# Optimization experiments

Measured on AMD Instinct MI355X. Metric: run time of the kernel, lower is better.

## Reference

```python
import jax, jax.numpy as jnp
import numpy as np

N_NODES = 8000
N_EDGES = 64000
HEADS = 8
OUT_C = 512
NEG_SLOPE = 0.2
EPS = 1e-16


def setup_inputs() -> dict:
    key = jax.random.key(0)
    ks = jax.random.split(key, 8)
    x = jax.random.normal(ks[0], (N_NODES, 128), dtype=jnp.float32)
    edge_index = jax.random.randint(ks[1], (2, N_EDGES), 0, N_NODES, dtype=jnp.int64)
    W_gat = jax.random.normal(ks[2], (128, HEADS * OUT_C), dtype=jnp.float32) * 0.05
    b_gat = jax.random.normal(ks[3], (HEADS * OUT_C,), dtype=jnp.float32) * 0.05
    att_src = jax.random.normal(ks[4], (HEADS, OUT_C), dtype=jnp.float32) * 0.05
    att_dst = jax.random.normal(ks[5], (HEADS, OUT_C), dtype=jnp.float32) * 0.05
    W_lin = jax.random.normal(ks[6], (HEADS * OUT_C, 512), dtype=jnp.float32) * 0.02
    b_lin = jax.random.normal(ks[7], (512,), dtype=jnp.float32) * 0.02
    return {"x": x, "edge_index": edge_index, "W_gat": W_gat, "b_gat": b_gat,
            "att_src": att_src, "att_dst": att_dst, "W_lin": W_lin, "b_lin": b_lin}


def reference(x, edge_index, W_gat, b_gat, att_src, att_dst, W_lin, b_lin):
    N = x.shape[0]
    # shared linear projection (PyG GATConv single-tensor input): [N, H, C]
    h = (x @ W_gat).reshape(N, HEADS, OUT_C)
    # add self loops (PyG default add_self_loops=True)
    loop = jnp.arange(N, dtype=edge_index.dtype)
    src = jnp.concatenate([edge_index[0], loop])  # source j
    dst = jnp.concatenate([edge_index[1], loop])  # destination i
    # per-node attention logits: [N, H]
    a_src = jnp.einsum('nhc,hc->nh', h, att_src)
    a_dst = jnp.einsum('nhc,hc->nh', h, att_dst)
    # edge logits, leaky relu
    e = jax.nn.leaky_relu(a_src[src] + a_dst[dst], NEG_SLOPE)  # [E, H]
    # softmax over edges sharing a destination
    emax = jax.ops.segment_max(e, dst, num_segments=N)
    ez = jnp.exp(e - emax[dst])
    denom = jax.ops.segment_sum(ez, dst, num_segments=N)
    alpha = ez / (denom[dst] + EPS)  # [E, H]
    # weighted scatter-add of source features
    msg = h[src] * alpha[:, :, None]  # [E, H, C]
    agg = jax.ops.segment_sum(msg, dst, num_segments=N)  # [N, H, C]
    gat_out = agg.reshape(N, HEADS * OUT_C) + b_gat
    return gat_out @ W_lin + b_lin
```

## Files before the change

### kernel.cpp

```cpp
#include <hip/hip_runtime.h>
#include <hip/hip_bf16.h>
#include <type_traits>

#define NN   8000
#define NE   64000
#define NE2  72000
#define NH   8
#define OC   512
#define HC   4096
#define KIN  128
#define NOUT 512
#define YW   1024
#define NEG_SLOPE 0.2f

using bf16 = __hip_bfloat16;
typedef float  f32x4  __attribute__((ext_vector_type(4)));
typedef __bf16 bf16x8 __attribute__((ext_vector_type(8)));

static __device__ __forceinline__ void gld_lds16(const bf16* g, bf16* l){
    __builtin_amdgcn_global_load_lds(
        (const __attribute__((address_space(1))) unsigned int*)g,
        (__attribute__((address_space(3))) unsigned int*)l, 16, 0, 0);
}

struct Acc24 { f32x4 a[2][4]; };

static __device__ __forceinline__ void gemm64x128(
    const bf16* __restrict__ A, int lda, const bf16* __restrict__ BT, int ldb,
    int K, bf16* sA, bf16* sB, int tid, Acc24& acc)
{
    const int lane = tid & 63;
    const int w    = tid >> 6;
    const int wm   = w >> 1, wn = w & 1;
    const int m16  = lane & 15, q = lane >> 4;
    const int rA = tid >> 2,  kA = (tid & 3) * 8;
    const int cB0 = tid, cB1 = 256 + tid;
    const int rB0 = cB0 >> 2, kB0 = (cB0 & 3) * 8;
    const int rB1 = cB1 >> 2, kB1 = (cB1 & 3) * 8;
    const size_t gA  = (size_t)rA  * lda + kA;
    const size_t gB0 = (size_t)rB0 * ldb + kB0;
    const size_t gB1 = (size_t)rB1 * ldb + kB1;

    #pragma unroll
    for (int i=0;i<2;++i)
        #pragma unroll
        for (int j=0;j<4;++j)
            #pragma unroll
            for (int r=0;r<4;++r) acc.a[i][j][r] = 0.f;

    gld_lds16(A  + gA,  sA + tid*8);
    gld_lds16(BT + gB0, sB + cB0*8);
    gld_lds16(BT + gB1, sB + cB1*8);
    __syncthreads();

    const int nIter = K / 32;
    for (int it = 0; it < nIter; ++it){
        const int cur = it & 1, nxt = cur ^ 1;
        bf16x8 af[2], bfr[4];
        #pragma unroll
        for (int i=0;i<2;++i)
            af[i]  = *(const bf16x8*)(const void*)(sA + cur*64*32 + ((wm*32 + i*16 + m16)*32 + q*8));
        #pragma unroll
        for (int j=0;j<4;++j)
            bfr[j] = *(const bf16x8*)(const void*)(sB + cur*128*32 + ((wn*64 + j*16 + m16)*32 + q*8));
        if (it + 1 < nIter){
            int ko = (it+1) * 32;
            gld_lds16(A  + gA  + ko, sA + nxt*64*32 + tid*8);
            gld_lds16(BT + gB0 + ko, sB + nxt*128*32 + cB0*8);
            gld_lds16(BT + gB1 + ko, sB + nxt*128*32 + cB1*8);
        }
        #pragma unroll
        for (int i=0;i<2;++i)
            #pragma unroll
            for (int j=0;j<4;++j)
                acc.a[i][j] = __builtin_amdgcn_mfma_f32_16x16x32_bf16(af[i], bfr[j], acc.a[i][j], 0, 0, 0);
        __syncthreads();
    }
}

#define TCVT_NB   2048
#define VSRC_BASE 2048
#define CNT_BASE  2176
#define PHA_NB    2458

__global__ __launch_bounds__(256) void k_phaseA(
    const float* __restrict__ W_lin, const float* __restrict__ b_gat,
    const float* __restrict__ W_gat,
    const float* __restrict__ att_src, const float* __restrict__ att_dst,
    const int* __restrict__ eidx,
    bf16* __restrict__ Wl_t, float* __restrict__ b_eff,
    bf16* __restrict__ Wg_bf, float* __restrict__ v,
    int* __restrict__ counts)
{
    __shared__ __align__(16) float smem[32*33 + 32];
    const int bid = blockIdx.x;
    const int tid = threadIdx.x;

    if (bid < TCVT_NB){
        float (*t)[33] = (float(*)[33])smem;
        float* bpart = smem + 32*33;
        if (tid < 32) bpart[tid] = 0.f;
        __syncthreads();
        int tx = tid & 31, ty = tid >> 5;
        int n0 = (bid & 15) * 32, k0 = (bid >> 4) * 32;
        float pb = 0.f;
        #pragma unroll
        for (int i=0;i<4;++i){
            int k = k0 + ty + 8*i;
            float val = W_lin[(size_t)k*NOUT + n0 + tx];
            t[ty+8*i][tx] = val;
            pb = fmaf(b_gat[k], val, pb);
        }
        atomicAdd(&bpart[tx], pb);
        __syncthreads();
        #pragma unroll
        for (int i=0;i<4;++i)
            Wl_t[(size_t)(n0+ty+8*i)*HC + k0+tx] = __float2bfloat16(t[tx][ty+8*i]);
        if (tid < 32) atomicAdd(b_eff + n0 + tid, bpart[tid]);
    } else if (bid < CNT_BASE){
        int k = bid - VSRC_BASE;
        int lane = tid & 63, g = tid >> 6;
        for (int hh = g; hh < NH; hh += 4){
            const float* wp = W_gat + (size_t)k*HC + hh*OC;
            bf16*        wb = Wg_bf + (size_t)k*HC + hh*OC;
            const float* as = att_src + hh*OC;
            const float* ad = att_dst + hh*OC;
            float ss = 0.f, sd = 0.f;
            #pragma unroll
            for (int c0=0; c0<OC; c0+=64){
                float wv = wp[c0+lane];
                wb[c0+lane] = __float2bfloat16(wv);
                ss = fmaf(wv, as[c0+lane], ss);
                sd = fmaf(wv, ad[c0+lane], sd);
            }
            #pragma unroll
            for (int off=32; off; off>>=1){
                ss += __shfl_down(ss, off);
                sd += __shfl_down(sd, off);
            }
            if (lane == 0){
                v[k*16 + hh]     = ss;
                v[k*16 + 8 + hh] = sd;
            }
        }
    } else {
        int e = (bid - CNT_BASE)*256 + tid;
        if (e < NE2){
            int dst = (e < NE) ? eidx[NE + e] : (e - NE);
            atomicAdd(&counts[dst], 1);
        }
    }
}

__global__ __launch_bounds__(256) void k_phaseB(
    const bf16* __restrict__ Wl_t, const bf16* __restrict__ Wg_bf,
    bf16* __restrict__ WcT,
    const int* __restrict__ counts, int* __restrict__ offsets)
{
    __shared__ __align__(16) char smem_raw[24576];
    __shared__ int part[256];
    const int bid = blockIdx.x;
    const int tid = threadIdx.x;

    if (bid == 64){
        int t = tid;
        int base = t*32;
        int s = 0;
        for (int u=0;u<32;++u){ int i = base+u; if (i<NN) s += counts[i]; }
        part[t] = s;
        __syncthreads();
        for (int off=1; off<256; off<<=1){
            int vv = (t>=off) ? part[t-off] : 0;
            __syncthreads();
            part[t] += vv;
            __syncthreads();
        }
        int run = (t==0) ? 0 : part[t-1];
        for (int u=0;u<32;++u){
            int i = base+u;
            if (i<NN){ offsets[i] = run; run += counts[i]; }
        }
        if (t == 255) offsets[NN] = run;
        return;
    }

    bf16* sA = (bf16*)smem_raw;
    bf16* sB = (bf16*)(smem_raw + 8192);
    const int head = bid >> 3, mt = bid & 7;
    const bf16* A  = Wl_t  + head*OC + (size_t)(mt*64)*HC;
    const bf16* BT = Wg_bf + head*OC;
    Acc24 acc;
    gemm64x128(A, HC, BT, HC, OC, sA, sB, tid, acc);
    const int lane = tid & 63;
    const int w = tid >> 6, wm = w >> 1, wn = w & 1;
    const int m16 = lane & 15, q = lane >> 4;
    #pragma unroll
    for (int i=0;i<2;++i){
        int o_base = mt*64 + wm*32 + i*16 + q*4;
        #pragma unroll
        for (int j=0;j<4;++j){
            int col = head*KIN + wn*64 + j*16 + m16;
            #pragma unroll
            for (int r=0;r<4;++r)
                WcT[(size_t)(o_base + r)*YW + col] = __float2bfloat16(acc.a[i][j][r]);
        }
    }
}

#define FILL_NB 282
#define PHC_NB  782

__global__ __launch_bounds__(256) void k_phaseC(
    const int* __restrict__ eidx, const int* __restrict__ offsets,
    int* __restrict__ cursors, int* __restrict__ esrc,
    const float* __restrict__ x, const float* __restrict__ v,
    float* __restrict__ a_src, float* __restrict__ a_dst)
{
    __shared__ __align__(16) float smem[16*132*2];
    const int bid = blockIdx.x;
    const int tid = threadIdx.x;

    if (bid < FILL_NB){
        int e = bid*256 + tid;
        if (e < NE2){
            int src, dst;
            if (e < NE){ src = eidx[e]; dst = eidx[NE+e]; } else { src = dst = e - NE; }
            int pos = atomicAdd(&cursors[dst], 1);
            esrc[offsets[dst] + pos] = src;
        }
        return;
    }
    float (*xs)[132] = (float(*)[132])smem;
    float (*vt)[132] = (float(*)[132])(smem + 16*132);
    int node0 = (bid - FILL_NB) * 16;
    {
        const float* xg = x + (size_t)node0*KIN;
        int row = tid >> 4, co = (tid & 15) * 8;
        float4 v0 = *(const float4*)(xg + row*KIN + co);
        float4 v1 = *(const float4*)(xg + row*KIN + co + 4);
        *(float4*)&xs[row][co]     = v0;
        *(float4*)&xs[row][co + 4] = v1;
    }
    {
        int base = tid*8;
        #pragma unroll
        for (int j=0;j<8;++j){
            int idx = base + j;
            vt[idx & 15][idx >> 4] = v[idx];
        }
    }
    __syncthreads();
    int ln = tid >> 4, o = tid & 15;
    float acc = 0.f;
    #pragma unroll
    for (int k0=0;k0<KIN;k0+=4){
        float4 xv = *(const float4*)&xs[ln][k0];
        float4 vv = *(const float4*)&vt[o][k0];
        acc += xv.x*vv.x + xv.y*vv.y + xv.z*vv.z + xv.w*vv.w;
    }
    int node = node0 + ln;
    if (o < 8) a_src[node*NH + o]     = acc;
    else       a_dst[node*NH + o - 8] = acc;
}

__global__ __launch_bounds__(256) void k_agg(const int* __restrict__ offs,
    const int* __restrict__ esrc, const float* __restrict__ a_src,
    const float* __restrict__ a_dst, const float* __restrict__ x,
    bf16* __restrict__ Y)
{
    int node = blockIdx.x*4 + (threadIdx.x >> 6);
    int lane = threadIdx.x & 63;
    int s0 = offs[node], s1 = offs[node+1];
    int g = lane >> 3, h = lane & 7;
    float adl = a_dst[node*NH + h];
    float m = -1e30f, sum = 0.f;
    for (int e = s0 + g; e < s1; e += 8){
        float l = a_src[esrc[e]*NH + h] + adl;
        l = l > 0.f ? l : NEG_SLOPE*l;
        float mn = fmaxf(m, l);
        sum = sum*__expf(m - mn) + __expf(l - mn);
        m = mn;
    }
    #pragma unroll
    for (int d=8; d<64; d<<=1){
        float mo = __shfl_xor(m, d);
        float so = __shfl_xor(sum, d);
        float mn = fmaxf(m, mo);
        sum = sum*__expf(m - mn) + so*__expf(mo - mn);
        m = mn;
    }
    float inv = 1.f / (sum + 1e-16f);
    float acc[16];
    #pragma unroll
    for (int j=0;j<16;++j) acc[j] = 0.f;
    for (int s=s0; s<s1; ++s){
        int src = esrc[s];
        float wl = 0.f;
        if (lane < 8){
            float l = a_src[src*NH + lane] + adl;
            l = l > 0.f ? l : NEG_SLOPE*l;
            wl = __expf(l - m) * inv;
        }
        float2 xv = *(const float2*)(x + (size_t)src*KIN + lane*2);
        #pragma unroll
        for (int hh=0; hh<8; ++hh){
            float wh = __shfl(wl, hh);
            acc[hh*2]   = fmaf(wh, xv.x, acc[hh*2]);
            acc[hh*2+1] = fmaf(wh, xv.y, acc[hh*2+1]);
        }
    }
    bf16* yp = Y + (size_t)node*YW + lane*2;
    #pragma unroll
    for (int hh=0; hh<8; ++hh){
        bf16 b0 = __float2bfloat16(acc[hh*2]);
        bf16 b1 = __float2bfloat16(acc[hh*2+1]);
        ushort2 pk;
        pk.x = *(unsigned short*)&b0;
        pk.y = *(unsigned short*)&b1;
        *reinterpret_cast<ushort2*>(yp + hh*KIN) = pk;
    }
}

__global__ __launch_bounds__(256) void k_gemm64(
    const bf16* __restrict__ A, const bf16* __restrict__ BT,
    const float* __restrict__ b_eff, const float* __restrict__ b_lin,
    float* __restrict__ C)
{
    __shared__ __align__(16) char smem_raw[24576];
    bf16* sA = (bf16*)smem_raw;
    bf16* sB = (bf16*)(smem_raw + 8192);
    const int tid = threadIdx.x;
    int m0 = blockIdx.x * 64;
    int n0 = blockIdx.y * 128;
    Acc24 acc;
    gemm64x128(A + (size_t)m0*YW, YW, BT + (size_t)n0*YW, YW, YW, sA, sB, tid, acc);
    const int lane = tid & 63;
    const int w = tid >> 6, wm = w >> 1, wn = w & 1;
    const int m16 = lane & 15, q = lane >> 4;
    #pragma unroll
    for (int i=0;i<2;++i){
        int row_base = m0 + wm*32 + i*16 + q*4;
        #pragma unroll
        for (int j=0;j<4;++j){
            int col = n0 + wn*64 + j*16 + m16;
            float bval = b_eff[col] + b_lin[col];
            #pragma unroll
            for (int r=0;r<4;++r)
                C[(size_t)(row_base + r)*NOUT + col] = acc.a[i][j][r] + bval;
        }
    }
}

extern "C" void kernel_launch(void* const* d_in, const int* in_sizes, int n_in,
                              void* d_out, int out_size, void* d_ws, size_t ws_size,
                              hipStream_t stream)
{
    const float* x       = (const float*)d_in[0];
    const int*   eidx    = (const int*)  d_in[1];
    const float* W_gat   = (const float*)d_in[2];
    const float* b_gat   = (const float*)d_in[3];
    const float* att_src = (const float*)d_in[4];
    const float* att_dst = (const float*)d_in[5];
    const float* W_lin   = (const float*)d_in[6];
    const float* b_lin   = (const float*)d_in[7];
    float* out = (float*)d_out;

    char* p = (char*)d_ws;
    auto alloc = [&](size_t bytes){ void* r = (void*)p; p += (bytes + 255) & ~(size_t)255; return r; };
    bf16*  Wg_bf  = (bf16*) alloc((size_t)KIN*HC*2);
    bf16*  Wl_t   = (bf16*) alloc((size_t)NOUT*HC*2);
    bf16*  WcT    = (bf16*) alloc((size_t)NOUT*YW*2);
    bf16*  Ybuf   = (bf16*) alloc((size_t)NN*YW*2);
    float* v      = (float*)alloc((size_t)KIN*16*4);
    float* a_src  = (float*)alloc((size_t)NN*NH*4);
    float* a_dst  = (float*)alloc((size_t)NN*NH*4);
    int*   offs   = (int*)  alloc((size_t)(NN+1)*4);
    int*   esrc   = (int*)  alloc((size_t)NE2*4);
    int*   counts = (int*)  alloc((size_t)NN*4);
    int*   cursors= (int*)  alloc((size_t)NN*4);
    float* b_eff  = (float*)alloc((size_t)NOUT*4);
    if ((size_t)(p - (char*)d_ws) > ws_size) return;

    hipMemsetAsync(counts, 0, (size_t)2*NN*4 + NOUT*4, stream);
    k_phaseA<<<PHA_NB, 256, 0, stream>>>(W_lin, b_gat, W_gat, att_src, att_dst,
                                         eidx, Wl_t, b_eff, Wg_bf, v, counts);
    k_phaseB<<<65, 256, 0, stream>>>(Wl_t, Wg_bf, WcT, counts, offs);
    k_phaseC<<<PHC_NB, 256, 0, stream>>>(eidx, offs, cursors, esrc, x, v, a_src, a_dst);
    k_agg<<<NN/4, 256, 0, stream>>>(offs, esrc, a_src, a_dst, x, Ybuf);
    k_gemm64<<<dim3(NN/64, NOUT/128), 256, 0, stream>>>(Ybuf, WcT, b_eff, b_lin, out);
}
```

Baseline: 147.5 us.

## Fuse W_lin transpose and bias folding into phase-B weight-combine GEMM

Removes the separate W_lin transpose/bf16 conversion pass (2048 blocks) from phase A. Phase B now reads fp32 W_lin directly, converting and transposing it into LDS inside the GEMM loop. b_gat is appended as row 128 of the bf16 W_gat buffer so the bias contribution b_gat·W_lin falls out of the same GEMM and is atomically added into b_eff. This cuts a full write and re-read of the intermediate transposed weights, at the cost of non-pipelined scalar LDS transposes, bf16 rounding of the bias product, and 96 GEMM blocks each with only 16 k-steps.

Result: no change. 146.7 us (-0.5%).

```diff
diff --git a/kernel.cpp b/kernel.cpp
--- a/kernel.cpp
+++ b/kernel.cpp
@@ -78,51 +78,27 @@
     }
 }
 
-#define TCVT_NB   2048
-#define VSRC_BASE 2048
-#define CNT_BASE  2176
-#define PHA_NB    2458
+#define VSRC_NB   128
+#define BCVT_BASE 128
+#define CNT_BASE  130
+#define PHA_NB    412
 
 __global__ __launch_bounds__(256) void k_phaseA(
-    const float* __restrict__ W_lin, const float* __restrict__ b_gat,
-    const float* __restrict__ W_gat,
+    const float* __restrict__ b_gat, const float* __restrict__ W_gat,
     const float* __restrict__ att_src, const float* __restrict__ att_dst,
     const int* __restrict__ eidx,
-    bf16* __restrict__ Wl_t, float* __restrict__ b_eff,
-    bf16* __restrict__ Wg_bf, float* __restrict__ v,
+    bf16* __restrict__ Wg_ext, float* __restrict__ v,
     int* __restrict__ counts)
 {
-    __shared__ __align__(16) float smem[32*33 + 32];
     const int bid = blockIdx.x;
     const int tid = threadIdx.x;
 
-    if (bid < TCVT_NB){
-        float (*t)[33] = (float(*)[33])smem;
-        float* bpart = smem + 32*33;
-        if (tid < 32) bpart[tid] = 0.f;
-        __syncthreads();
-        int tx = tid & 31, ty = tid >> 5;
-        int n0 = (bid & 15) * 32, k0 = (bid >> 4) * 32;
-        float pb = 0.f;
-        #pragma unroll
-        for (int i=0;i<4;++i){
-            int k = k0 + ty + 8*i;
-            float val = W_lin[(size_t)k*NOUT + n0 + tx];
-            t[ty+8*i][tx] = val;
-            pb = fmaf(b_gat[k], val, pb);
-        }
-        atomicAdd(&bpart[tx], pb);
-        __syncthreads();
-        #pragma unroll
-        for (int i=0;i<4;++i)
-            Wl_t[(size_t)(n0+ty+8*i)*HC + k0+tx] = __float2bfloat16(t[tx][ty+8*i]);
-        if (tid < 32) atomicAdd(b_eff + n0 + tid, bpart[tid]);
-    } else if (bid < CNT_BASE){
-        int k = bid - VSRC_BASE;
+    if (bid < VSRC_NB){
+        int k = bid;
         int lane = tid & 63, g = tid >> 6;
         for (int hh = g; hh < NH; hh += 4){
             const float* wp = W_gat + (size_t)k*HC + hh*OC;
-            bf16*        wb = Wg_bf + (size_t)k*HC + hh*OC;
+            bf16*        wb = Wg_ext + (size_t)k*HC + hh*OC;
             const float* as = att_src + hh*OC;
             const float* ad = att_dst + hh*OC;
             float ss = 0.f, sd = 0.f;
@@ -143,6 +119,14 @@
                 v[k*16 + 8 + hh] = sd;
             }
         }
+    } else if (bid < CNT_BASE){
+        int idx = (bid - BCVT_BASE)*2048 + tid*8;
+        float4 v0 = *(const float4*)(b_gat + idx);
+        float4 v1 = *(const float4*)(b_gat + idx + 4);
+        bf16x8 o;
+        o[0]=(__bf16)v0.x; o[1]=(__bf16)v0.y; o[2]=(__bf16)v0.z; o[3]=(__bf16)v0.w;
+        o[4]=(__bf16)v1.x; o[5]=(__bf16)v1.y; o[6]=(__bf16)v1.z; o[7]=(__bf16)v1.w;
+        *(bf16x8*)(void*)(Wg_ext + (size_t)128*HC + idx) = o;
     } else {
         int e = (bid - CNT_BASE)*256 + tid;
         if (e < NE2){
@@ -152,17 +136,20 @@
     }
 }
 
+#define PB_GEMM_NB 96
+
 __global__ __launch_bounds__(256) void k_phaseB(
-    const bf16* __restrict__ Wl_t, const bf16* __restrict__ Wg_bf,
-    bf16* __restrict__ WcT,
+    const bf16* __restrict__ Wg_ext, const float* __restrict__ W_lin,
+    bf16* __restrict__ WcT, float* __restrict__ b_eff,
     const int* __restrict__ counts, int* __restrict__ offsets)
 {
-    __shared__ __align__(16) char smem_raw[24576];
+    __shared__ __align__(16) bf16 sA[64*32];
+    __shared__ __align__(16) bf16 sB[128*32];
     __shared__ int part[256];
     const int bid = blockIdx.x;
     const int tid = threadIdx.x;
 
-    if (bid == 64){
+    if (bid == PB_GEMM_NB){
         int t = tid;
         int base = t*32;
         int s = 0;
@@ -184,25 +171,81 @@
         return;
     }
 
-    bf16* sA = (bf16*)smem_raw;
-    bf16* sB = (bf16*)(smem_raw + 8192);
-    const int head = bid >> 3, mt = bid & 7;
-    const bf16* A  = Wl_t  + head*OC + (size_t)(mt*64)*HC;
-    const bf16* BT = Wg_bf + head*OC;
-    Acc24 acc;
-    gemm64x128(A, HC, BT, HC, OC, sA, sB, tid, acc);
+    const int head = bid / 12;
+    const int rem  = bid % 12;
+    const int m0   = (rem >> 2) * 64;
+    const int n0   = (rem & 3) * 128;
     const int lane = tid & 63;
     const int w = tid >> 6, wm = w >> 1, wn = w & 1;
     const int m16 = lane & 15, q = lane >> 4;
+
+    const int rA = tid >> 2, kA = (tid & 3) * 8;
+    const int arow = min(m0 + rA, 128);
+    const bf16* Abase = Wg_ext + (size_t)arow*HC + head*OC + kA;
+
+    f32x4 acc[2][4];
+    #pragma unroll
+    for (int i=0;i<2;++i)
+        #pragma unroll
+        for (int j=0;j<4;++j)
+            #pragma unroll
+            for (int r=0;r<4;++r) acc[i][j][r] = 0.f;
+
+    for (int kc = 0; kc < OC; kc += 32){
+        __syncthreads();
+        gld_lds16(Abase + kc, sA + tid*8);
+        #pragma unroll
+        for (int u=0; u<4; ++u){
+            int idx = tid*4 + u;
+            int r    = idx >> 5;
+            int gcol = (idx & 31) * 4;
+            const float* src = W_lin + (size_t)(head*OC + kc + r)*NOUT + n0 + gcol;
+            float4 vv = *(const float4*)src;
+            sB[(gcol+0)*32 + r] = __float2bfloat16(vv.x);
+            sB[(gcol+1)*32 + r] = __float2bfloat16(vv.y);
+            sB[(gcol+2)*32 + r] = __float2bfloat16(vv.z);
+            sB[(gcol+3)*32 + r] = __float2bfloat16(vv.w);
+        }
+        __syncthreads();
+        bf16x8 af[2], bfr[4];
+        #pragma unroll
+        for (int i=0;i<2;++i)
+            af[i]  = *(const bf16x8*)(const void*)(sA + ((wm*32 + i*16 + m16)*32 + q*8));
+        #pragma unroll
+        for (int j=0;j<4;++j)
+            bfr[j] = *(const bf16x8*)(const void*)(sB + ((wn*64 + j*16 + m16)*32 + q*8));
+        #pragma unroll
+        for (int i=0;i<2;++i)
+            #pragma unroll
+            for (int j=0;j<4;++j)
+                acc[i][j] = __builtin_amdgcn_mfma_f32_16x16x32_bf16(af[i], bfr[j], acc[i][j], 0, 0, 0);
+    }
+
     #pragma unroll
     for (int i=0;i<2;++i){
-        int o_base = mt*64 + wm*32 + i*16 + q*4;
+        int row_base = m0 + wm*32 + i*16 + q*4;
         #pragma unroll
         for (int j=0;j<4;++j){
-            int col = head*KIN + wn*64 + j*16 + m16;
-            #pragma unroll
-            for (int r=0;r<4;++r)
-                WcT[(size_t)(o_base + r)*YW + col] = __float2bfloat16(acc.a[i][j][r]);
+            int col = n0 + wn*64 + j*16 + m16;
+            if (row_base + 3 < 128){
+                ushort4 pk;
+                bf16 b0 = __float2bfloat16(acc[i][j][0]);
+                bf16 b1 = __float2bfloat16(acc[i][j][1]);
+                bf16 b2 = __float2bfloat16(acc[i][j][2]);
+                bf16 b3 = __float2bfloat16(acc[i][j][3]);
+                pk.x = *(unsigned short*)&b0; pk.y = *(unsigned short*)&b1;
+                pk.z = *(unsigned short*)&b2; pk.w = *(unsigned short*)&b3;
+                *reinterpret_cast<ushort4*>(WcT + (size_t)col*YW + head*KIN + row_base) = pk;
+            } else {
+                #pragma unroll
+                for (int r=0;r<4;++r){
+                    int row = row_base + r;
+                    if (row < 128)
+                        WcT[(size_t)col*YW + head*KIN + row] = __float2bfloat16(acc[i][j][r]);
+                    else if (row == 128)
+                        atomicAdd(b_eff + col, acc[i][j][r]);
+                }
+            }
         }
     }
 }
@@ -367,8 +410,7 @@
 
     char* p = (char*)d_ws;
     auto alloc = [&](size_t bytes){ void* r = (void*)p; p += (bytes + 255) & ~(size_t)255; return r; };
-    bf16*  Wg_bf  = (bf16*) alloc((size_t)KIN*HC*2);
-    bf16*  Wl_t   = (bf16*) alloc((size_t)NOUT*HC*2);
+    bf16*  Wg_ext = (bf16*) alloc((size_t)129*HC*2);
     bf16*  WcT    = (bf16*) alloc((size_t)NOUT*YW*2);
     bf16*  Ybuf   = (bf16*) alloc((size_t)NN*YW*2);
     float* v      = (float*)alloc((size_t)KIN*16*4);
@@ -382,9 +424,9 @@
     if ((size_t)(p - (char*)d_ws) > ws_size) return;
 
     hipMemsetAsync(counts, 0, (size_t)2*NN*4 + NOUT*4, stream);
-    k_phaseA<<<PHA_NB, 256, 0, stream>>>(W_lin, b_gat, W_gat, att_src, att_dst,
-                                         eidx, Wl_t, b_eff, Wg_bf, v, counts);
-    k_phaseB<<<65, 256, 0, stream>>>(Wl_t, Wg_bf, WcT, counts, offs);
+    k_phaseA<<<PHA_NB, 256, 0, stream>>>(b_gat, W_gat, att_src, att_dst,
+                                         eidx, Wg_ext, v, counts);
+    k_phaseB<<<PB_GEMM_NB + 1, 256, 0, stream>>>(Wg_ext, W_lin, WcT, b_eff, counts, offs);
     k_phaseC<<<PHC_NB, 256, 0, stream>>>(eidx, offs, cursors, esrc, x, v, a_src, a_dst);
     k_agg<<<NN/4, 256, 0, stream>>>(offs, esrc, a_src, a_dst, x, Ybuf);
     k_gemm64<<<dim3(NN/64, NOUT/128), 256, 0, stream>>>(Ybuf, WcT, b_eff, b_lin, out);
```
